# Kernel tuning notes

Measured on AMD Instinct MI355X. Metric: run time of the kernel, lower is better.

## Reference

```python
import jax, jax.numpy as jnp
import numpy as np

D_MODEL = 2048
N_HEADS = 16
HEAD_DIM = D_MODEL // N_HEADS  # 128
MAX_SEQ = 2048
ROPE_BASE = 10000.0


def _rope(t, start_pos):
    # t: (B, S, Hn, head_dim); standard interleaved-pair RoPE
    B, S, Hn, hd = t.shape
    inv_freq = 1.0 / (ROPE_BASE ** (jnp.arange(0, hd, 2, dtype=jnp.float32) / hd))  # (hd/2,)
    pos = jnp.arange(start_pos, start_pos + S, dtype=jnp.float32)                    # (S,)
    ang = pos[:, None] * inv_freq[None, :]                                           # (S, hd/2)
    cos = jnp.cos(ang)[None, :, None, :]
    sin = jnp.sin(ang)[None, :, None, :]
    x1 = t[..., 0::2]
    x2 = t[..., 1::2]
    o1 = x1 * cos - x2 * sin
    o2 = x1 * sin + x2 * cos
    return jnp.stack([o1, o2], axis=-1).reshape(t.shape)


def setup_inputs() -> dict:
    key = jax.random.key(0)
    ks = jax.random.split(key, 9)
    s = 1.0 / np.sqrt(D_MODEL)
    return {
        "x": jax.random.normal(ks[0], (4, 2048, D_MODEL), dtype=jnp.float32),
        "wq": jax.random.uniform(ks[1], (D_MODEL, D_MODEL), jnp.float32, -s, s),
        "bq": jax.random.uniform(ks[2], (D_MODEL,), jnp.float32, -s, s),
        "wk": jax.random.uniform(ks[3], (D_MODEL, HEAD_DIM), jnp.float32, -s, s),
        "bk": jax.random.uniform(ks[4], (HEAD_DIM,), jnp.float32, -s, s),
        "wv": jax.random.uniform(ks[5], (D_MODEL, HEAD_DIM), jnp.float32, -s, s),
        "bv": jax.random.uniform(ks[6], (HEAD_DIM,), jnp.float32, -s, s),
        "wo": jax.random.uniform(ks[7], (D_MODEL, D_MODEL), jnp.float32, -s, s),
        "bo": jax.random.uniform(ks[8], (D_MODEL,), jnp.float32, -s, s),
    }


def reference(x, wq, bq, wk, bk, wv, bv, wo, bo):
    # Prefill path: start_pos=0, kv_cache=None.
    B, S, D = x.shape
    q = (x @ wq + bq).reshape(B, S, N_HEADS, HEAD_DIM)  # (B,S,H,hd)
    k = (x @ wk + bk).reshape(B, S, 1, HEAD_DIM)        # (B,S,1,hd) shared KV head
    v = (x @ wv + bv).reshape(B, S, 1, HEAD_DIM)
    q = _rope(q, 0)
    k = _rope(k, 0)
    qh = q.transpose(0, 2, 1, 3)          # (B,H,S,hd)
    kh = k.transpose(0, 2, 1, 3)          # (B,1,S,hd)  -> kv_cache entry
    vh = v.transpose(0, 2, 1, 3)
    scores = jnp.einsum("bhqd,bkd->bhqk", qh, kh[:, 0]) / jnp.sqrt(
        jnp.asarray(HEAD_DIM, dtype=x.dtype))
    # original buffer: tril(ones) with zeros replaced by -inf -> allowed positions get +1
    tril = jnp.tril(jnp.ones((S, S), dtype=bool))
    mask = jnp.where(tril, jnp.asarray(1.0, x.dtype), jnp.asarray(-jnp.inf, x.dtype))
    scores = scores + mask[None, None, :, :]
    p = jax.nn.softmax(scores, axis=-1)                 # (B,H,S,S)
    attn = jnp.einsum("bhqk,bkd->bhqd", p, vh[:, 0])    # (B,H,S,hd)
    out = attn.transpose(0, 2, 1, 3).reshape(B, S, D) @ wo + bo
    return (out, kh, vh)
```

## Files before the change

kernel.cpp:

```cpp
#include <hip/hip_runtime.h>
#include <hip/hip_bf16.h>
#include <cstdint>
#include <cstddef>

#define SEQ 2048
#define DM 2048
#define NHEADS 16
#define HD 128
#define NTOK 8192
#define BATCH 4

typedef __bf16 bf16_t;
typedef bf16_t bf16x8 __attribute__((ext_vector_type(8)));
typedef float f32x4 __attribute__((ext_vector_type(4)));

__device__ __forceinline__ void async_copy16(const bf16_t* g, bf16_t* l) {
  __builtin_amdgcn_global_load_lds(
      (const __attribute__((address_space(1))) unsigned int*)g,
      (__attribute__((address_space(3))) unsigned int*)l, 16, 0, 0);
}

__device__ __forceinline__ void store_out(float* p, float v)  { *p = v; }
__device__ __forceinline__ void store_out(bf16_t* p, float v) { *p = (bf16_t)v; }

#define SB  __builtin_amdgcn_sched_barrier(0)
#define BAR __builtin_amdgcn_s_barrier()
#define LGKM0 asm volatile("s_waitcnt lgkmcnt(0)" ::: "memory")


__global__ void convert_x_bf16(const float* __restrict__ in, bf16_t* __restrict__ out, int n4) {
  int i = blockIdx.x * 256 + threadIdx.x;
  if (i >= n4) return;
  float4 v = ((const float4*)in)[i];
  union { ushort4 u; bf16_t b[4]; } o;
  o.b[0] = (bf16_t)v.x; o.b[1] = (bf16_t)v.y; o.b[2] = (bf16_t)v.z; o.b[3] = (bf16_t)v.w;
  *(ushort4*)(out + (size_t)i * 4) = o.u;
}

__global__ void transpose_f32_to_bf16(const float* __restrict__ in, bf16_t* __restrict__ out,
                                      int R, int C) {
  __shared__ float tile[32][33];
  int c0 = blockIdx.x * 32, r0 = blockIdx.y * 32;
  int tx = threadIdx.x & 31, ty = threadIdx.x >> 5;
  for (int i = ty; i < 32; i += 8) tile[i][tx] = in[(size_t)(r0 + i) * C + c0 + tx];
  __syncthreads();
  for (int i = ty; i < 32; i += 8) out[(size_t)(c0 + i) * R + r0 + tx] = (bf16_t)tile[tx][i];
}

template <typename OutT>
__global__ __launch_bounds__(256) void gemm_bt(const bf16_t* __restrict__ A,
                                               const bf16_t* __restrict__ Bt,
                                               const float* __restrict__ bias,
                                               OutT* __restrict__ C, int M, int N, int K) {
  __shared__ bf16_t As[128 * 32];
  __shared__ bf16_t Bs[128 * 32];
  const int tid = threadIdx.x;
  const int lane = tid & 63;
  const int wv = tid >> 6;
  const int wi = wv >> 1, wj = wv & 1;
  const int quad = lane >> 4, l16 = lane & 15;
  const size_t m0 = (size_t)blockIdx.x * 128, n0 = (size_t)blockIdx.y * 128;

  f32x4 acc[4][4] = {};

  const bf16_t* ag = A + (m0 + (tid >> 2)) * K + (tid & 3) * 8;
  const bf16_t* bg = Bt + (n0 + (tid >> 2)) * K + (tid & 3) * 8;
  bf16_t* asd = As + tid * 8;
  bf16_t* bsd = Bs + tid * 8;
  const int nk = K >> 5;
  for (int kt = 0; kt < nk; kt++) {
    async_copy16(ag, asd);
    async_copy16(ag + (size_t)64 * K, asd + 64 * 32);
    async_copy16(bg, bsd);
    async_copy16(bg + (size_t)64 * K, bsd + 64 * 32);
    ag += 32; bg += 32;
    __syncthreads();
    bf16x8 af[4], bf[4];
#pragma unroll
    for (int mt = 0; mt < 4; mt++)
      af[mt] = *(const bf16x8*)(As + (wi * 64 + mt * 16 + l16) * 32 + quad * 8);
#pragma unroll
    for (int nt = 0; nt < 4; nt++)
      bf[nt] = *(const bf16x8*)(Bs + (wj * 64 + nt * 16 + l16) * 32 + quad * 8);
#pragma unroll
    for (int mt = 0; mt < 4; mt++)
#pragma unroll
      for (int nt = 0; nt < 4; nt++)
        acc[mt][nt] = __builtin_amdgcn_mfma_f32_16x16x32_bf16(af[mt], bf[nt], acc[mt][nt], 0, 0, 0);
    __syncthreads();
  }
#pragma unroll
  for (int nt = 0; nt < 4; nt++) {
    float bb = bias[n0 + wj * 64 + nt * 16 + l16];
#pragma unroll
    for (int mt = 0; mt < 4; mt++) {
      size_t row = m0 + wi * 64 + mt * 16 + quad * 4;
      size_t col = n0 + wj * 64 + nt * 16 + l16;
#pragma unroll
      for (int r = 0; r < 4; r++) store_out(&C[(row + r) * N + col], acc[mt][nt][r] + bb);
    }
  }
}

template <typename OutT>
__global__ __launch_bounds__(512, 2) void gemm256(const bf16_t* __restrict__ A,
                                                  const bf16_t* __restrict__ Bt,
                                                  const float* __restrict__ bias,
                                                  OutT* __restrict__ C, int M, int N, int K) {
  extern __shared__ char smem_raw[];
  bf16_t* As_ = (bf16_t*)smem_raw;
  bf16_t* Bs_ = As_ + 32768;

  const int tid = threadIdx.x;
  const int lane = tid & 63;
  const int wv = tid >> 6;
  const int wr = wv >> 2, wc = wv & 3;
  const int quad = lane >> 4, l16 = lane & 15;

  const int bid = blockIdx.x;
  const int g = (bid & 7) * 32 + (bid >> 3);
  const size_t m0 = (size_t)(g >> 3) * 256;
  const size_t n0 = (size_t)(g & 7) * 256;

  auto mkrow = [](int s) { int rp = s >> 3; int Cc = (s & 7) ^ (rp & 7); return rp * 2 + (Cc >> 2); };
  auto mkkc  = [](int s) { int rp = s >> 3; int Cc = (s & 7) ^ (rp & 7); return (Cc & 3) * 8; };
  const bf16_t* pA0 = A  + (size_t)(m0 + mkrow(tid)) * K + mkkc(tid);
  const bf16_t* pA1 = A  + (size_t)(m0 + mkrow(tid + 512)) * K + mkkc(tid + 512);
  const bf16_t* pB0 = Bt + (size_t)(n0 + mkrow(tid)) * K + mkkc(tid);
  const bf16_t* pB1 = Bt + (size_t)(n0 + mkrow(tid + 512)) * K + mkkc(tid + 512);

#define STAGE_A(SLOT, KH, KT) do { \
    async_copy16(pA0 + (size_t)(KT) * 64 + (KH) * 32, As_ + (SLOT) * 16384 + (KH) * 8192 + tid * 8); \
    async_copy16(pA1 + (size_t)(KT) * 64 + (KH) * 32, As_ + (SLOT) * 16384 + (KH) * 8192 + (tid + 512) * 8); \
  } while (0)
#define STAGE_B(SLOT, KH, KT) do { \
    async_copy16(pB0 + (size_t)(KT) * 64 + (KH) * 32, Bs_ + (SLOT) * 16384 + (KH) * 8192 + tid * 8); \
    async_copy16(pB1 + (size_t)(KT) * 64 + (KH) * 32, Bs_ + (SLOT) * 16384 + (KH) * 8192 + (tid + 512) * 8); \
  } while (0)

  int aoffs[8], boffs[4];
#pragma unroll
  for (int mi = 0; mi < 8; mi++) {
    int row = wr * 128 + mi * 16 + l16;
    int rp = row >> 1, Cc = (row & 1) * 4 + quad;
    aoffs[mi] = rp * 64 + (Cc ^ (rp & 7)) * 8;
  }
#pragma unroll
  for (int ni = 0; ni < 4; ni++) {
    int row = wc * 64 + ni * 16 + l16;
    int rp = row >> 1, Cc = (row & 1) * 4 + quad;
    boffs[ni] = rp * 64 + (Cc ^ (rp & 7)) * 8;
  }

  f32x4 acc[8][4] = {};
  bf16x8 afr[8], b0, b1;

#define LOAD_A(SLOT, KS) do { _Pragma("unroll") \
    for (int mi = 0; mi < 8; mi++) afr[mi] = *(const bf16x8*)(As_ + (SLOT) * 16384 + (KS) * 8192 + aoffs[mi]); \
  } while (0)
#define LOAD_B2(SLOT, KS, NF0) do { \
    b0 = *(const bf16x8*)(Bs_ + (SLOT) * 16384 + (KS) * 8192 + boffs[NF0]); \
    b1 = *(const bf16x8*)(Bs_ + (SLOT) * 16384 + (KS) * 8192 + boffs[(NF0) + 1]); \
  } while (0)
#define MFMA16(NF0) do { __builtin_amdgcn_s_setprio(1); _Pragma("unroll") \
    for (int mi = 0; mi < 8; mi++) { \
      acc[mi][NF0] = __builtin_amdgcn_mfma_f32_16x16x32_bf16(afr[mi], b0, acc[mi][NF0], 0, 0, 0); \
      acc[mi][(NF0) + 1] = __builtin_amdgcn_mfma_f32_16x16x32_bf16(afr[mi], b1, acc[mi][(NF0) + 1], 0, 0, 0); \
    } __builtin_amdgcn_s_setprio(0); } while (0)

  const int NI = K >> 7;

  STAGE_A(0, 0, 0); STAGE_B(0, 0, 0);
  STAGE_A(0, 1, 0); STAGE_B(0, 1, 0);
  STAGE_A(1, 0, 1); STAGE_B(1, 0, 1);
  asm volatile("s_waitcnt vmcnt(0)" ::: "memory");
  SB; BAR; SB;

#pragma unroll 1
  for (int j = 0; j < NI; j++) {
    const int last = (j == NI - 1);
    LOAD_A(0, 0); LOAD_B2(0, 0, 0);
    STAGE_A(1, 1, 2 * j + 1);
    SB; BAR; LGKM0; SB; MFMA16(0); SB; BAR;
    LOAD_B2(0, 0, 2);
    STAGE_B(1, 1, 2 * j + 1);
    SB; BAR; LGKM0; SB; MFMA16(2); SB; BAR;
    LOAD_A(0, 1); LOAD_B2(0, 1, 0);
    if (!last) STAGE_A(0, 0, 2 * j + 2);
    SB; BAR; LGKM0; SB; MFMA16(0); SB; BAR;
    LOAD_B2(0, 1, 2);
    if (!last) STAGE_B(0, 0, 2 * j + 2);
    SB;
    if (!last) { asm volatile("s_waitcnt vmcnt(4)" ::: "memory"); }
    else       { asm volatile("s_waitcnt vmcnt(0)" ::: "memory"); }
    BAR; LGKM0; SB; MFMA16(2); SB; BAR;
    LOAD_A(1, 0); LOAD_B2(1, 0, 0);
    if (!last) STAGE_A(0, 1, 2 * j + 2);
    SB; BAR; LGKM0; SB; MFMA16(0); SB; BAR;
    LOAD_B2(1, 0, 2);
    if (!last) STAGE_B(0, 1, 2 * j + 2);
    SB; BAR; LGKM0; SB; MFMA16(2); SB; BAR;
    LOAD_A(1, 1); LOAD_B2(1, 1, 0);
    if (!last) STAGE_A(1, 0, 2 * j + 3);
    SB; BAR; LGKM0; SB; MFMA16(0); SB; BAR;
    LOAD_B2(1, 1, 2);
    if (!last) STAGE_B(1, 0, 2 * j + 3);
    SB;
    if (!last) { asm volatile("s_waitcnt vmcnt(4)" ::: "memory"); }
    else       { asm volatile("s_waitcnt vmcnt(0)" ::: "memory"); }
    BAR; LGKM0; SB; MFMA16(2); SB; BAR;
  }

#pragma unroll
  for (int ni = 0; ni < 4; ni++) {
    size_t col = n0 + wc * 64 + ni * 16 + l16;
    float bb = bias[col];
#pragma unroll
    for (int mi = 0; mi < 8; mi++) {
      size_t row = m0 + wr * 128 + mi * 16 + quad * 4;
#pragma unroll
      for (int r = 0; r < 4; r++) store_out(&C[(row + r) * N + col], acc[mi][ni][r] + bb);
    }
  }
#undef STAGE_A
#undef STAGE_B
#undef LOAD_A
#undef LOAD_B2
#undef MFMA16
}

#define ROPE_C 0.14391156831212787f
#define ATT_SCALE 0.1275174462517703f

__global__ void rope_q_kernel(bf16_t* __restrict__ q) {
  int idx = blockIdx.x * 256 + threadIdx.x;
  int tok = idx >> 8;
  int c0 = (idx & 255) * 8;
  int s = tok & (SEQ - 1);
  int d0 = c0 & (HD - 1);
  union { uint4 u; ushort us[8]; } v;
  v.u = *(const uint4*)(q + (size_t)tok * DM + c0);
  float x[8];
#pragma unroll
  for (int j = 0; j < 8; j++) x[j] = __uint_as_float((uint32_t)v.us[j] << 16);
#pragma unroll
  for (int j = 0; j < 4; j++) {
    int i = (d0 >> 1) + j;
    float fr = __expf(-(float)i * ROPE_C);
    float ang = (float)s * fr;
    float sn, cs; __sincosf(ang, &sn, &cs);
    float o1 = (x[2 * j] * cs - x[2 * j + 1] * sn) * ATT_SCALE;
    float o2 = (x[2 * j] * sn + x[2 * j + 1] * cs) * ATT_SCALE;
    x[2 * j] = o1; x[2 * j + 1] = o2;
  }
  union { uint4 u; ushort us[8]; } w;
#pragma unroll
  for (int j = 0; j < 8; j++) {
    union { float f; uint32_t u; } t; t.f = x[j];
    uint32_t r = (t.u + 0x7fff + ((t.u >> 16) & 1)) >> 16;
    w.us[j] = (ushort)r;
  }
  *(uint4*)(q + (size_t)tok * DM + c0) = w.u;
}

__global__ void rope_kv_kernel(const float* __restrict__ kvf, float* __restrict__ kh,
                               float* __restrict__ vh, bf16_t* __restrict__ kbf) {
  int idx = blockIdx.x * 256 + threadIdx.x;
  int t = idx >> 6;
  int i = idx & 63;
  int s = t & (SEQ - 1);
  const float* base = kvf + (size_t)t * 256;
  float x1 = base[2 * i], x2 = base[2 * i + 1];
  float fr = __expf(-(float)i * ROPE_C);
  float ang = (float)s * fr;
  float sn, cs; __sincosf(ang, &sn, &cs);
  float k1 = x1 * cs - x2 * sn, k2 = x1 * sn + x2 * cs;
  size_t o = (size_t)t * HD + 2 * i;
  kh[o] = k1; kh[o + 1] = k2;
  kbf[o] = (bf16_t)k1; kbf[o + 1] = (bf16_t)k2;
  vh[o] = base[128 + 2 * i];
  vh[o + 1] = base[128 + 2 * i + 1];
}

__global__ void transpose_v_kernel(const float* __restrict__ kvf, bf16_t* __restrict__ vT) {
  __shared__ float tile[32][33];
  int b = blockIdx.z;
  int s0 = blockIdx.x * 32, d0 = blockIdx.y * 32;
  int tx = threadIdx.x & 31, ty = threadIdx.x >> 5;
  for (int i = ty; i < 32; i += 8)
    tile[i][tx] = kvf[(size_t)(b * SEQ + s0 + i) * 256 + 128 + d0 + tx];
  __syncthreads();
  for (int i = ty; i < 32; i += 8)
    vT[(size_t)b * HD * SEQ + (size_t)(d0 + i) * SEQ + s0 + tx] = (bf16_t)tile[tx][i];
}

__global__ __launch_bounds__(256, 2) void flash_attn_kernel(const bf16_t* __restrict__ Q,
                                                            const bf16_t* __restrict__ Kb,
                                                            const bf16_t* __restrict__ VT,
                                                            bf16_t* __restrict__ O) {
  __shared__ bf16_t Ks[2][64 * 128];
  __shared__ bf16_t Vs[2][64 * 128];
  const int tid = threadIdx.x;
  const int lane = tid & 63;
  const int wv = tid >> 6;
  const int quad = lane >> 4, l16 = lane & 15;
  const int pr = blockIdx.x, h = blockIdx.y, b = blockIdx.z;

  const bf16_t* kbase = Kb + (size_t)b * SEQ * HD;
  const bf16_t* vbase = VT + (size_t)b * HD * SEQ;

  int cur = 0;
#pragma unroll
  for (int i = 0; i < 4; i++) {
    int p = i * 256 + tid;
    int kr = p >> 4, kc = (p & 15) ^ (kr & 15);
    async_copy16(kbase + (size_t)kr * HD + kc * 8, &Ks[0][p * 8]);
    int vr = p >> 3, vc = (p & 7) ^ (vr & 7);
    async_copy16(vbase + (size_t)vr * SEQ + vc * 8, &Vs[0][p * 8]);
  }

#pragma unroll 1
  for (int ph = 0; ph < 2; ph++) {
    const int qt = ph ? pr : 15 - pr;
    const int nkt = 2 * qt + 2;

    bf16x8 qf[2][4];
#pragma unroll
    for (int nt = 0; nt < 2; nt++) {
      size_t qrow = (size_t)b * SEQ + qt * 128 + wv * 32 + nt * 16 + l16;
      const bf16_t* qp = Q + qrow * DM + h * HD + quad * 8;
#pragma unroll
      for (int ks = 0; ks < 4; ks++) qf[nt][ks] = *(const bf16x8*)(qp + ks * 32);
    }

    f32x4 oacc[8][2] = {};
    float l2[2] = {0.f, 0.f};

#pragma unroll 1
    for (int kt = 0; kt < nkt; kt++) {
      asm volatile("s_waitcnt lgkmcnt(0)" ::: "memory");
      SB; BAR; SB;

      const int has_next = !(ph == 1 && kt == nkt - 1);
      if (has_next) {
        const int k0n = (kt + 1 < nkt) ? (kt + 1) * 64 : 0;
        bf16_t* kd = &Ks[cur ^ 1][0];
        bf16_t* vd = &Vs[cur ^ 1][0];
#pragma unroll
        for (int i = 0; i < 4; i++) {
          int p = i * 256 + tid;
          int kr = p >> 4, kc = (p & 15) ^ (kr & 15);
          async_copy16(kbase + (size_t)(k0n + kr) * HD + kc * 8, kd + p * 8);
          int vr = p >> 3, vc = (p & 7) ^ (vr & 7);
          async_copy16(vbase + (size_t)vr * SEQ + k0n + vc * 8, vd + p * 8);
        }
        asm volatile("s_waitcnt vmcnt(8)" ::: "memory");
      } else {
        asm volatile("s_waitcnt vmcnt(0)" ::: "memory");
      }
      SB; BAR; SB;

      const bf16_t* KsC = &Ks[cur][0];
      const bf16_t* VsC = &Vs[cur][0];

      f32x4 sa[4][2] = {};
#pragma unroll
      for (int ks = 0; ks < 4; ks++) {
        bf16x8 ak[4];
#pragma unroll
        for (int mt = 0; mt < 4; mt++) {
          int row = mt * 16 + l16;
          int c = (ks * 4 + quad) ^ l16;
          ak[mt] = *(const bf16x8*)(KsC + (row * 16 + c) * 8);
        }
        __builtin_amdgcn_s_setprio(1);
#pragma unroll
        for (int mt = 0; mt < 4; mt++)
#pragma unroll
          for (int nt = 0; nt < 2; nt++)
            sa[mt][nt] = __builtin_amdgcn_mfma_f32_16x16x32_bf16(ak[mt], qf[nt][ks], sa[mt][nt], 0, 0, 0);
        __builtin_amdgcn_s_setprio(0);
      }

      if (kt >= 2 * qt) {
        const int k0c = kt * 64;
#pragma unroll
        for (int mt = 0; mt < 4; mt++)
#pragma unroll
          for (int nt = 0; nt < 2; nt++) {
            int kg0 = k0c + mt * 16 + quad * 4;
            int qg = qt * 128 + wv * 32 + nt * 16 + l16;
#pragma unroll
            for (int r = 0; r < 4; r++)
              if (kg0 + r > qg) sa[mt][nt][r] = -INFINITY;
          }
      }

      bf16x8 bp[2][2];
#pragma unroll
      for (int nt = 0; nt < 2; nt++) {
        float rs = 0.f;
#pragma unroll
        for (int mt = 0; mt < 4; mt++)
#pragma unroll
          for (int r = 0; r < 4; r++) {
            float pv = exp2f(sa[mt][nt][r]);
            sa[mt][nt][r] = pv;
            rs += pv;
          }
        {
          float a0 = rs, a1 = rs;
          asm("v_permlane16_swap_b32 %0, %1" : "+v"(a0), "+v"(a1));
          rs = a0 + a1;
          float c0 = rs, c1 = rs;
          asm("v_permlane32_swap_b32 %0, %1" : "+v"(c0), "+v"(c1));
          rs = c0 + c1;
        }
        l2[nt] += rs;

        uint32_t d0[4], d1[4];
#pragma unroll
        for (int m = 0; m < 4; m++) {
          asm("v_cvt_pk_bf16_f32 %0, %1, %2" : "=v"(d0[m]) : "v"(sa[m][nt][0]), "v"(sa[m][nt][1]));
          asm("v_cvt_pk_bf16_f32 %0, %1, %2" : "=v"(d1[m]) : "v"(sa[m][nt][2]), "v"(sa[m][nt][3]));
        }
#pragma unroll
        for (int ks = 0; ks < 2; ks++) {
          uint32_t w0 = d0[2 * ks], w2 = d0[2 * ks + 1];
          uint32_t w1 = d1[2 * ks], w3 = d1[2 * ks + 1];
          asm("v_permlane32_swap_b32 %0, %1" : "+v"(w0), "+v"(w2));
          asm("v_permlane16_swap_b32 %0, %1" : "+v"(w0), "+v"(w2));
          asm("v_permlane32_swap_b32 %0, %1" : "+v"(w1), "+v"(w3));
          asm("v_permlane16_swap_b32 %0, %1" : "+v"(w1), "+v"(w3));
          union { uint32_t u[4]; bf16x8 v; } pk_;
          pk_.u[0] = w0; pk_.u[1] = w1; pk_.u[2] = w2; pk_.u[3] = w3;
          bp[nt][ks] = pk_.v;
        }
      }

#pragma unroll
      for (int ks = 0; ks < 2; ks++)
#pragma unroll
        for (int dm = 0; dm < 8; dm++) {
          int row = dm * 16 + l16;
          int c = (ks * 4 + quad) ^ (row & 7);
          bf16x8 av = *(const bf16x8*)(VsC + (row * 8 + c) * 8);
          __builtin_amdgcn_s_setprio(1);
#pragma unroll
          for (int nt = 0; nt < 2; nt++)
            oacc[dm][nt] = __builtin_amdgcn_mfma_f32_16x16x32_bf16(av, bp[nt][ks], oacc[dm][nt], 0, 0, 0);
          __builtin_amdgcn_s_setprio(0);
        }

      cur ^= 1;
    }

    float inv[2];
#pragma unroll
    for (int nt = 0; nt < 2; nt++) inv[nt] = 1.f / l2[nt];
#pragma unroll
    for (int dm = 0; dm < 8; dm++)
#pragma unroll
      for (int nt = 0; nt < 2; nt++) {
        size_t row = (size_t)b * SEQ + qt * 128 + wv * 32 + nt * 16 + l16;
        size_t col = (size_t)h * HD + dm * 16 + quad * 4;
        union { ushort4 u; bf16_t bb[4]; } pk;
#pragma unroll
        for (int r = 0; r < 4; r++) pk.bb[r] = (bf16_t)(oacc[dm][nt][r] * inv[nt]);
        *(ushort4*)(O + row * DM + col) = pk.u;
      }
  }
}


extern "C" void kernel_launch(void* const* d_in, const int* in_sizes, int n_in,
                              void* d_out, int out_size, void* d_ws, size_t ws_size,
                              hipStream_t stream) {
  const float* x  = (const float*)d_in[0];
  const float* wq = (const float*)d_in[1];
  const float* bq = (const float*)d_in[2];
  const float* wk = (const float*)d_in[3];
  const float* bk = (const float*)d_in[4];
  const float* wv = (const float*)d_in[5];
  const float* bv = (const float*)d_in[6];
  const float* wo = (const float*)d_in[7];
  const float* bo = (const float*)d_in[8];
  char* ws = (char*)d_ws;

  bf16_t* xbf  = (bf16_t*)(ws);
  bf16_t* qbf  = (bf16_t*)(ws + 33554432ull);
  bf16_t* wqT  = (bf16_t*)(ws + 67108864ull);
  bf16_t* woT  = (bf16_t*)(ws + 75497472ull);
  bf16_t* wkvT = (bf16_t*)(ws + 83886080ull);
  float*  kvf  = (float* )(ws + 84934656ull);
  bf16_t* kbf  = (bf16_t*)(ws + 93323264ull);
  bf16_t* vT   = (bf16_t*)(ws + 95420416ull);
  float*  bkv  = (float* )(ws + 97517568ull);
  bf16_t* attn = xbf;

  float* out = (float*)d_out;
  float* kh  = out + 16777216ull;
  float* vh  = kh + 1048576ull;

  hipFuncSetAttribute((const void*)gemm256<bf16_t>, hipFuncAttributeMaxDynamicSharedMemorySize, 131072);
  hipFuncSetAttribute((const void*)gemm256<float>,  hipFuncAttributeMaxDynamicSharedMemorySize, 131072);

  hipMemcpyAsync(bkv,       bk, 128 * sizeof(float), hipMemcpyDeviceToDevice, stream);
  hipMemcpyAsync(bkv + 128, bv, 128 * sizeof(float), hipMemcpyDeviceToDevice, stream);

  convert_x_bf16<<<16384, 256, 0, stream>>>(x, xbf, 4194304);
  transpose_f32_to_bf16<<<dim3(64, 64), 256, 0, stream>>>(wq, wqT, 2048, 2048);
  transpose_f32_to_bf16<<<dim3(64, 64), 256, 0, stream>>>(wo, woT, 2048, 2048);
  transpose_f32_to_bf16<<<dim3(4, 64), 256, 0, stream>>>(wk, wkvT, 2048, 128);
  transpose_f32_to_bf16<<<dim3(4, 64), 256, 0, stream>>>(wv, wkvT + 128 * 2048, 2048, 128);

  gemm256<bf16_t><<<256, 512, 131072, stream>>>(xbf, wqT, bq, qbf, 8192, 2048, 2048);
  gemm_bt<float ><<<dim3(64, 2), 256, 0, stream>>>(xbf, wkvT, bkv, kvf, 8192, 256, 2048);

  rope_q_kernel<<<8192, 256, 0, stream>>>(qbf);
  rope_kv_kernel<<<2048, 256, 0, stream>>>(kvf, kh, vh, kbf);
  transpose_v_kernel<<<dim3(64, 4, 4), 256, 0, stream>>>(kvf, vT);

  flash_attn_kernel<<<dim3(8, 16, 4), 256, 0, stream>>>(qbf, kbf, vT, attn);

  gemm256<float><<<256, 512, 131072, stream>>>(attn, woT, bo, out, 8192, 2048, 2048);
}
```

Before: 485.4 us.

## Fuse Q RoPE into attention Q load and merge small prep kernels

Q RoPE and scaling now happen inside the flash attention kernel while the Q fragments are loaded. This removes the separate rope_q pass, which read and wrote the full Q tensor. The weight transposes, the KV RoPE and the V transpose are merged into fewer launches, and the two bias memcpys are dropped by passing bk and bv directly. The attention loop's synchronisation is also moved: it now waits on all loads and barriers at the end of each iteration instead of the start, which may reduce overlap of the next tile's prefetch with compute.

```diff
diff --git a/kernel.cpp b/kernel.cpp
--- a/kernel.cpp
+++ b/kernel.cpp
@@ -23,9 +23,15 @@
 __device__ __forceinline__ void store_out(float* p, float v)  { *p = v; }
 __device__ __forceinline__ void store_out(bf16_t* p, float v) { *p = (bf16_t)v; }
 
+__device__ __forceinline__ ushort bf16_rne(float f) {
+  union { float f; uint32_t u; } t; t.f = f;
+  return (ushort)((t.u + 0x7fff + ((t.u >> 16) & 1)) >> 16);
+}
+
 #define SB  __builtin_amdgcn_sched_barrier(0)
 #define BAR __builtin_amdgcn_s_barrier()
 #define LGKM0 asm volatile("s_waitcnt lgkmcnt(0)" ::: "memory")
+#define VM0 asm volatile("s_waitcnt vmcnt(0)" ::: "memory")
 
 
 __global__ void convert_x_bf16(const float* __restrict__ in, bf16_t* __restrict__ out, int n4) {
@@ -37,21 +43,35 @@
   *(ushort4*)(out + (size_t)i * 4) = o.u;
 }
 
-__global__ void transpose_f32_to_bf16(const float* __restrict__ in, bf16_t* __restrict__ out,
-                                      int R, int C) {
+__global__ void transpose_qo(const float* __restrict__ wq, const float* __restrict__ wo,
+                             bf16_t* __restrict__ wqT, bf16_t* __restrict__ woT) {
   __shared__ float tile[32][33];
+  const float* in = blockIdx.z ? wo : wq;
+  bf16_t* out = blockIdx.z ? woT : wqT;
   int c0 = blockIdx.x * 32, r0 = blockIdx.y * 32;
   int tx = threadIdx.x & 31, ty = threadIdx.x >> 5;
-  for (int i = ty; i < 32; i += 8) tile[i][tx] = in[(size_t)(r0 + i) * C + c0 + tx];
+  for (int i = ty; i < 32; i += 8) tile[i][tx] = in[(size_t)(r0 + i) * 2048 + c0 + tx];
   __syncthreads();
-  for (int i = ty; i < 32; i += 8) out[(size_t)(c0 + i) * R + r0 + tx] = (bf16_t)tile[tx][i];
-}
-
-template <typename OutT>
-__global__ __launch_bounds__(256) void gemm_bt(const bf16_t* __restrict__ A,
-                                               const bf16_t* __restrict__ Bt,
-                                               const float* __restrict__ bias,
-                                               OutT* __restrict__ C, int M, int N, int K) {
+  for (int i = ty; i < 32; i += 8) out[(size_t)(c0 + i) * 2048 + r0 + tx] = (bf16_t)tile[tx][i];
+}
+
+__global__ void transpose_wkv(const float* __restrict__ wk, const float* __restrict__ wv,
+                              bf16_t* __restrict__ wkvT) {
+  __shared__ float tile[32][33];
+  const float* in = blockIdx.z ? wv : wk;
+  bf16_t* out = wkvT + (size_t)blockIdx.z * 128 * 2048;
+  int c0 = blockIdx.x * 32, r0 = blockIdx.y * 32;
+  int tx = threadIdx.x & 31, ty = threadIdx.x >> 5;
+  for (int i = ty; i < 32; i += 8) tile[i][tx] = in[(size_t)(r0 + i) * 128 + c0 + tx];
+  __syncthreads();
+  for (int i = ty; i < 32; i += 8) out[(size_t)(c0 + i) * 2048 + r0 + tx] = (bf16_t)tile[tx][i];
+}
+
+__global__ __launch_bounds__(256) void gemm_bt_kv(const bf16_t* __restrict__ A,
+                                                  const bf16_t* __restrict__ Bt,
+                                                  const float* __restrict__ bk,
+                                                  const float* __restrict__ bv,
+                                                  float* __restrict__ C, int M, int N, int K) {
   __shared__ bf16_t As[128 * 32];
   __shared__ bf16_t Bs[128 * 32];
   const int tid = threadIdx.x;
@@ -91,13 +111,13 @@
   }
 #pragma unroll
   for (int nt = 0; nt < 4; nt++) {
-    float bb = bias[n0 + wj * 64 + nt * 16 + l16];
+    size_t col = n0 + wj * 64 + nt * 16 + l16;
+    float bb = (col < 128) ? bk[col] : bv[col - 128];
 #pragma unroll
     for (int mt = 0; mt < 4; mt++) {
       size_t row = m0 + wi * 64 + mt * 16 + quad * 4;
-      size_t col = n0 + wj * 64 + nt * 16 + l16;
-#pragma unroll
-      for (int r = 0; r < 4; r++) store_out(&C[(row + r) * N + col], acc[mt][nt][r] + bb);
+#pragma unroll
+      for (int r = 0; r < 4; r++) C[(row + r) * N + col] = acc[mt][nt][r] + bb;
     }
   }
 }
@@ -173,7 +193,7 @@
   STAGE_A(0, 0, 0); STAGE_B(0, 0, 0);
   STAGE_A(0, 1, 0); STAGE_B(0, 1, 0);
   STAGE_A(1, 0, 1); STAGE_B(1, 0, 1);
-  asm volatile("s_waitcnt vmcnt(0)" ::: "memory");
+  VM0;
   SB; BAR; SB;
 
 #pragma unroll 1
@@ -192,7 +212,7 @@
     if (!last) STAGE_B(0, 0, 2 * j + 2);
     SB;
     if (!last) { asm volatile("s_waitcnt vmcnt(4)" ::: "memory"); }
-    else       { asm volatile("s_waitcnt vmcnt(0)" ::: "memory"); }
+    else       { VM0; }
     BAR; LGKM0; SB; MFMA16(2); SB; BAR;
     LOAD_A(1, 0); LOAD_B2(1, 0, 0);
     if (!last) STAGE_A(0, 1, 2 * j + 2);
@@ -207,7 +227,7 @@
     if (!last) STAGE_B(1, 0, 2 * j + 3);
     SB;
     if (!last) { asm volatile("s_waitcnt vmcnt(4)" ::: "memory"); }
-    else       { asm volatile("s_waitcnt vmcnt(0)" ::: "memory"); }
+    else       { VM0; }
     BAR; LGKM0; SB; MFMA16(2); SB; BAR;
   }
 
@@ -232,66 +252,37 @@
 #define ROPE_C 0.14391156831212787f
 #define ATT_SCALE 0.1275174462517703f
 
-__global__ void rope_q_kernel(bf16_t* __restrict__ q) {
-  int idx = blockIdx.x * 256 + threadIdx.x;
-  int tok = idx >> 8;
-  int c0 = (idx & 255) * 8;
-  int s = tok & (SEQ - 1);
-  int d0 = c0 & (HD - 1);
-  union { uint4 u; ushort us[8]; } v;
-  v.u = *(const uint4*)(q + (size_t)tok * DM + c0);
-  float x[8];
-#pragma unroll
-  for (int j = 0; j < 8; j++) x[j] = __uint_as_float((uint32_t)v.us[j] << 16);
-#pragma unroll
-  for (int j = 0; j < 4; j++) {
-    int i = (d0 >> 1) + j;
+__global__ void rope_kv_tv(const float* __restrict__ kvf, float* __restrict__ kh,
+                           float* __restrict__ vh, bf16_t* __restrict__ kbf,
+                           bf16_t* __restrict__ vT) {
+  int bid = blockIdx.x;
+  if (bid < 2048) {
+    int idx = bid * 256 + threadIdx.x;
+    int t = idx >> 6;
+    int i = idx & 63;
+    int s = t & (SEQ - 1);
+    const float* base = kvf + (size_t)t * 256;
+    float x1 = base[2 * i], x2 = base[2 * i + 1];
     float fr = __expf(-(float)i * ROPE_C);
     float ang = (float)s * fr;
     float sn, cs; __sincosf(ang, &sn, &cs);
-    float o1 = (x[2 * j] * cs - x[2 * j + 1] * sn) * ATT_SCALE;
-    float o2 = (x[2 * j] * sn + x[2 * j + 1] * cs) * ATT_SCALE;
-    x[2 * j] = o1; x[2 * j + 1] = o2;
-  }
-  union { uint4 u; ushort us[8]; } w;
-#pragma unroll
-  for (int j = 0; j < 8; j++) {
-    union { float f; uint32_t u; } t; t.f = x[j];
-    uint32_t r = (t.u + 0x7fff + ((t.u >> 16) & 1)) >> 16;
-    w.us[j] = (ushort)r;
-  }
-  *(uint4*)(q + (size_t)tok * DM + c0) = w.u;
-}
-
-__global__ void rope_kv_kernel(const float* __restrict__ kvf, float* __restrict__ kh,
-                               float* __restrict__ vh, bf16_t* __restrict__ kbf) {
-  int idx = blockIdx.x * 256 + threadIdx.x;
-  int t = idx >> 6;
-  int i = idx & 63;
-  int s = t & (SEQ - 1);
-  const float* base = kvf + (size_t)t * 256;
-  float x1 = base[2 * i], x2 = base[2 * i + 1];
-  float fr = __expf(-(float)i * ROPE_C);
-  float ang = (float)s * fr;
-  float sn, cs; __sincosf(ang, &sn, &cs);
-  float k1 = x1 * cs - x2 * sn, k2 = x1 * sn + x2 * cs;
-  size_t o = (size_t)t * HD + 2 * i;
-  kh[o] = k1; kh[o + 1] = k2;
-  kbf[o] = (bf16_t)k1; kbf[o + 1] = (bf16_t)k2;
-  vh[o] = base[128 + 2 * i];
-  vh[o + 1] = base[128 + 2 * i + 1];
-}
-
-__global__ void transpose_v_kernel(const float* __restrict__ kvf, bf16_t* __restrict__ vT) {
-  __shared__ float tile[32][33];
-  int b = blockIdx.z;
-  int s0 = blockIdx.x * 32, d0 = blockIdx.y * 32;
-  int tx = threadIdx.x & 31, ty = threadIdx.x >> 5;
-  for (int i = ty; i < 32; i += 8)
-    tile[i][tx] = kvf[(size_t)(b * SEQ + s0 + i) * 256 + 128 + d0 + tx];
-  __syncthreads();
-  for (int i = ty; i < 32; i += 8)
-    vT[(size_t)b * HD * SEQ + (size_t)(d0 + i) * SEQ + s0 + tx] = (bf16_t)tile[tx][i];
+    float k1 = x1 * cs - x2 * sn, k2 = x1 * sn + x2 * cs;
+    size_t o = (size_t)t * HD + 2 * i;
+    kh[o] = k1; kh[o + 1] = k2;
+    kbf[o] = (bf16_t)k1; kbf[o + 1] = (bf16_t)k2;
+    vh[o] = base[128 + 2 * i];
+    vh[o + 1] = base[128 + 2 * i + 1];
+  } else {
+    __shared__ float tile[32][33];
+    int t = bid - 2048;
+    int s0 = (t & 63) * 32, d0 = ((t >> 6) & 3) * 32, b = t >> 8;
+    int tx = threadIdx.x & 31, ty = threadIdx.x >> 5;
+    for (int i = ty; i < 32; i += 8)
+      tile[i][tx] = kvf[(size_t)(b * SEQ + s0 + i) * 256 + 128 + d0 + tx];
+    __syncthreads();
+    for (int i = ty; i < 32; i += 8)
+      vT[(size_t)b * HD * SEQ + (size_t)(d0 + i) * SEQ + s0 + tx] = (bf16_t)tile[tx][i];
+  }
 }
 
 __global__ __launch_bounds__(256, 2) void flash_attn_kernel(const bf16_t* __restrict__ Q,
@@ -318,6 +309,8 @@
     int vr = p >> 3, vc = (p & 7) ^ (vr & 7);
     async_copy16(vbase + (size_t)vr * SEQ + vc * 8, &Vs[0][p * 8]);
   }
+  VM0;
+  SB; BAR; SB;
 
 #pragma unroll 1
   for (int ph = 0; ph < 2; ph++) {
@@ -327,10 +320,27 @@
     bf16x8 qf[2][4];
 #pragma unroll
     for (int nt = 0; nt < 2; nt++) {
-      size_t qrow = (size_t)b * SEQ + qt * 128 + wv * 32 + nt * 16 + l16;
+      const int srow = qt * 128 + wv * 32 + nt * 16 + l16;
+      size_t qrow = (size_t)b * SEQ + srow;
       const bf16_t* qp = Q + qrow * DM + h * HD + quad * 8;
 #pragma unroll
-      for (int ks = 0; ks < 4; ks++) qf[nt][ks] = *(const bf16x8*)(qp + ks * 32);
+      for (int ks = 0; ks < 4; ks++) {
+        union { uint4 u4; ushort us[8]; } u;
+        u.u4 = *(const uint4*)(qp + ks * 32);
+        union { ushort us[8]; bf16x8 v; } w;
+#pragma unroll
+        for (int jj = 0; jj < 4; jj++) {
+          float x1 = __uint_as_float((uint32_t)u.us[2 * jj] << 16);
+          float x2 = __uint_as_float((uint32_t)u.us[2 * jj + 1] << 16);
+          int i = ks * 16 + quad * 4 + jj;
+          float fr = __expf(-(float)i * ROPE_C);
+          float ang = (float)srow * fr;
+          float sn, cs; __sincosf(ang, &sn, &cs);
+          w.us[2 * jj]     = bf16_rne((x1 * cs - x2 * sn) * ATT_SCALE);
+          w.us[2 * jj + 1] = bf16_rne((x1 * sn + x2 * cs) * ATT_SCALE);
+        }
+        qf[nt][ks] = w.v;
+      }
     }
 
     f32x4 oacc[8][2] = {};
@@ -338,9 +348,6 @@
 
 #pragma unroll 1
     for (int kt = 0; kt < nkt; kt++) {
-      asm volatile("s_waitcnt lgkmcnt(0)" ::: "memory");
-      SB; BAR; SB;
-
       const int has_next = !(ph == 1 && kt == nkt - 1);
       if (has_next) {
         const int k0n = (kt + 1 < nkt) ? (kt + 1) * 64 : 0;
@@ -354,11 +361,8 @@
           int vr = p >> 3, vc = (p & 7) ^ (vr & 7);
           async_copy16(vbase + (size_t)vr * SEQ + k0n + vc * 8, vd + p * 8);
         }
-        asm volatile("s_waitcnt vmcnt(8)" ::: "memory");
-      } else {
-        asm volatile("s_waitcnt vmcnt(0)" ::: "memory");
       }
-      SB; BAR; SB;
+      SB;
 
       const bf16_t* KsC = &Ks[cur][0];
       const bf16_t* VsC = &Vs[cur][0];
@@ -452,6 +456,9 @@
           __builtin_amdgcn_s_setprio(0);
         }
 
+      LGKM0;
+      VM0;
+      SB; BAR; SB;
       cur ^= 1;
     }
 
@@ -495,7 +502,6 @@
   float*  kvf  = (float* )(ws + 84934656ull);
   bf16_t* kbf  = (bf16_t*)(ws + 93323264ull);
   bf16_t* vT   = (bf16_t*)(ws + 95420416ull);
-  float*  bkv  = (float* )(ws + 97517568ull);
   bf16_t* attn = xbf;
 
   float* out = (float*)d_out;
@@ -505,21 +511,14 @@
   hipFuncSetAttribute((const void*)gemm256<bf16_t>, hipFuncAttributeMaxDynamicSharedMemorySize, 131072);
   hipFuncSetAttribute((const void*)gemm256<float>,  hipFuncAttributeMaxDynamicSharedMemorySize, 131072);
 
-  hipMemcpyAsync(bkv,       bk, 128 * sizeof(float), hipMemcpyDeviceToDevice, stream);
-  hipMemcpyAsync(bkv + 128, bv, 128 * sizeof(float), hipMemcpyDeviceToDevice, stream);
-
   convert_x_bf16<<<16384, 256, 0, stream>>>(x, xbf, 4194304);
-  transpose_f32_to_bf16<<<dim3(64, 64), 256, 0, stream>>>(wq, wqT, 2048, 2048);
-  transpose_f32_to_bf16<<<dim3(64, 64), 256, 0, stream>>>(wo, woT, 2048, 2048);
-  transpose_f32_to_bf16<<<dim3(4, 64), 256, 0, stream>>>(wk, wkvT, 2048, 128);
-  transpose_f32_to_bf16<<<dim3(4, 64), 256, 0, stream>>>(wv, wkvT + 128 * 2048, 2048, 128);
+  transpose_qo<<<dim3(64, 64, 2), 256, 0, stream>>>(wq, wo, wqT, woT);
+  transpose_wkv<<<dim3(4, 64, 2), 256, 0, stream>>>(wk, wv, wkvT);
 
   gemm256<bf16_t><<<256, 512, 131072, stream>>>(xbf, wqT, bq, qbf, 8192, 2048, 2048);
-  gemm_bt<float ><<<dim3(64, 2), 256, 0, stream>>>(xbf, wkvT, bkv, kvf, 8192, 256, 2048);
-
-  rope_q_kernel<<<8192, 256, 0, stream>>>(qbf);
-  rope_kv_kernel<<<2048, 256, 0, stream>>>(kvf, kh, vh, kbf);
-  transpose_v_kernel<<<dim3(64, 4, 4), 256, 0, stream>>>(kvf, vT);
+  gemm_bt_kv<<<dim3(64, 2), 256, 0, stream>>>(xbf, wkvT, bk, bv, kvf, 8192, 256, 2048);
+
+  rope_kv_tv<<<3072, 256, 0, stream>>>(kvf, kh, vh, kbf, vT);
 
   flash_attn_kernel<<<dim3(8, 16, 4), 256, 0, stream>>>(qbf, kbf, vT, attn);
 
```

Measured after the change: 463.5 us. 4.5% less time.
